# Kernel tuning notes

Measured on AMD Instinct MI355X. Metric: run time of the kernel, lower is better.

The kernel has to match this reference:

```python
import jax, jax.numpy as jnp
import numpy as np

N = 50000   # nodes
E = 800000  # edges (avg degree 16)
DIMS = [(128, 128), (128, 128), (128, 64)]  # (in, out) per SAGEConv layer
EPS_BN = 1e-5
EPS_NORM = 1e-12


def _make_layer(key, din, dout):
    k1, k2 = jax.random.split(key)
    s = 1.0 / np.sqrt(din)
    return (
        jax.random.normal(k1, (dout, din), jnp.float32) * s,  # Wl: neighbor linear
        jnp.zeros((dout,), jnp.float32),                      # bl
        jax.random.normal(k2, (dout, din), jnp.float32) * s,  # Wr: root linear (no bias in PyG)
        jnp.ones((dout,), jnp.float32),                       # bn gamma
        jnp.zeros((dout,), jnp.float32),                      # bn beta
        jnp.zeros((dout,), jnp.float32),                      # bn running mean
        jnp.ones((dout,), jnp.float32),                       # bn running var
    )


def setup_inputs() -> dict:
    key = jax.random.key(0)
    kx, ke, k0, k1, k2 = jax.random.split(key, 5)
    inp = {
        "x": jax.random.normal(kx, (N, 128), jnp.float32),
        "edge_index": jax.random.randint(ke, (2, E), 0, N, dtype=jnp.int32),
    }
    for i, (k, (din, dout)) in enumerate(zip([k0, k1, k2], DIMS)):
        Wl, bl, Wr, g, b, rm, rv = _make_layer(k, din, dout)
        inp.update({f"Wl{i}": Wl, f"bl{i}": bl, f"Wr{i}": Wr,
                    f"g{i}": g, f"b{i}": b, f"rm{i}": rm, f"rv{i}": rv})
    return inp


def _sage_conv(x, src, dst, Wl, bl, Wr):
    # mean aggregation of incoming messages: gather src features, scatter-add at dst
    agg = jax.ops.segment_sum(x[src], dst, num_segments=N)          # [N, din]
    deg = jax.ops.segment_sum(jnp.ones((src.shape[0],), x.dtype), dst, num_segments=N)
    mean = agg / jnp.maximum(deg, 1.0)[:, None]
    return mean @ Wl.T + bl + x @ Wr.T


def _bn_eval(x, g, b, rm, rv):
    return g * (x - rm) * jax.lax.rsqrt(rv + EPS_BN) + b


def reference(x, edge_index,
              Wl0, bl0, Wr0, g0, b0, rm0, rv0,
              Wl1, bl1, Wr1, g1, b1, rm1, rv1,
              Wl2, bl2, Wr2, g2, b2, rm2, rv2):
    src, dst = edge_index[0], edge_index[1]
    layers = [
        (Wl0, bl0, Wr0, g0, b0, rm0, rv0),
        (Wl1, bl1, Wr1, g1, b1, rm1, rv1),
        (Wl2, bl2, Wr2, g2, b2, rm2, rv2),
    ]
    h = x
    for i, (Wl, bl, Wr, g, b, rm, rv) in enumerate(layers):
        h = _bn_eval(_sage_conv(h, src, dst, Wl, bl, Wr), g, b, rm, rv)
        if i < len(layers) - 1:
            h = jax.nn.relu(h)  # dropout is identity in eval mode
    # F.normalize(p=2, dim=1)
    return h / jnp.maximum(jnp.linalg.norm(h, axis=1, keepdims=True), EPS_NORM)
```

## Files before the change

kernel.cpp:

```cpp
#include <hip/hip_runtime.h>
#include <hip/hip_bf16.h>

#define CDIV(a,b) (((a)+(b)-1)/(b))
#define NBUCK_MAX 512
#define FUSE_CAP 1536
#define CAPL     4096
#define AGGF_CAP 2048

typedef __attribute__((ext_vector_type(8))) short short8;
typedef __attribute__((ext_vector_type(4))) float f32x4;
typedef __attribute__((ext_vector_type(2))) float f32x2;

static __device__ __forceinline__ unsigned short f2bf(float f){
  union { float f; unsigned u; } v; v.f = f;
  unsigned r = v.u + 0x7fffu + ((v.u >> 16) & 1u);
  return (unsigned short)(r >> 16);
}
static __device__ __forceinline__ unsigned pack2(float lo, float hi){
  return (unsigned)f2bf(lo) | ((unsigned)f2bf(hi) << 16);
}
static __device__ __forceinline__ float bf2f(unsigned short s){
  union { unsigned u; float f; } v; v.u = ((unsigned)s) << 16; return v.f;
}
static __device__ __forceinline__ unsigned pk_fp8x4(float a, float b, float c, float d){
  int v = __builtin_amdgcn_cvt_pk_fp8_f32(a, b, 0, false);
  v = __builtin_amdgcn_cvt_pk_fp8_f32(c, d, v, true);
  return (unsigned)v;
}

#define ACCP16(v) { b0 += __builtin_amdgcn_cvt_pk_f32_fp8((int)v.x, false); \
                    b1 += __builtin_amdgcn_cvt_pk_f32_fp8((int)v.x, true);  \
                    b2 += __builtin_amdgcn_cvt_pk_f32_fp8((int)v.y, false); \
                    b3 += __builtin_amdgcn_cvt_pk_f32_fp8((int)v.y, true);  \
                    b4 += __builtin_amdgcn_cvt_pk_f32_fp8((int)v.z, false); \
                    b5 += __builtin_amdgcn_cvt_pk_f32_fp8((int)v.z, true);  \
                    b6 += __builtin_amdgcn_cvt_pk_f32_fp8((int)v.w, false); \
                    b7 += __builtin_amdgcn_cvt_pk_f32_fp8((int)v.w, true); }


struct WtpArgs {
  const float *W0, *W1, *bl, *g, *b, *rm, *rv;
  unsigned short* Bpk; float *sc; float *sh;
  int kblk, dout, do_bn, nblk, perm;
};

static __device__ __forceinline__ void wtp_one(const WtpArgs& a, int idx){
  int NB16 = a.kblk*32*a.dout;
  if (idx < NB16){
    int j = idx & 7, lane = (idx >> 3) & 63, rest = idx >> 9;
    int NT = a.dout >> 4;
    int nt = rest % NT, kk = rest / NT;
    int nn = nt*16 + (lane & 15);
    int k  = kk*32 + ((lane >> 4) * 8) + j;
    float v;
    if (k < 128){
      int kc = a.perm ? (((k & 7) << 4) | (k >> 3)) : k;
      v = a.W0[nn*128 + kc];
    } else {
      v = a.W1[nn*128 + (k - 128)];
    }
    a.Bpk[idx] = f2bf(v);
  } else if (a.do_bn && idx < NB16 + a.dout){
    int jj = idx - NB16;
    float s = a.g[jj] * rsqrtf(a.rv[jj] + 1e-5f);
    a.sc[jj] = s;
    a.sh[jj] = (a.bl[jj] - a.rm[jj]) * s + a.b[jj];
  }
}


__global__ __launch_bounds__(256) void k_prep(const float* __restrict__ x, int n4, unsigned* __restrict__ xb,
                                              unsigned* __restrict__ xq,
                                              const int* __restrict__ dst, int E,
                                              int* __restrict__ bcnt, int nbuck,
                                              int castBlocks, int histBlocks,
                                              WtpArgs a0, WtpArgs a1, WtpArgs a2, WtpArgs a3){
  __shared__ int s[NBUCK_MAX];
  int b = blockIdx.x, t = threadIdx.x;
  if (b < castBlocks){
    int i = b*256 + t;
    if (i < n4){
      float4 v = ((const float4*)x)[i];
      uint2 o; o.x = pack2(v.x, v.y); o.y = pack2(v.z, v.w);
      ((uint2*)xb)[i] = o;
      xq[i] = pk_fp8x4(v.x, v.y, v.z, v.w);
    }
    return;
  }
  b -= castBlocks;
  if (b < histBlocks){
    for (int i=t;i<nbuck;i+=256) s[i] = 0;
    __syncthreads();
    constexpr int EPT = 16;
    int e0 = b*256*EPT;
    #pragma unroll
    for (int i=0;i<EPT;i++){
      int e = e0 + i*256 + t;
      if (e < E) atomicAdd(&s[dst[e] >> 7], 1);
    }
    __syncthreads();
    for (int i=t;i<nbuck;i+=256){
      int c = s[i];
      if (c > 0) atomicAdd(&bcnt[i], c);
    }
    return;
  }
  b -= histBlocks;
  if (b < a0.nblk){ wtp_one(a0, b*256 + t); return; }
  b -= a0.nblk;
  if (b < a1.nblk){ wtp_one(a1, b*256 + t); return; }
  b -= a1.nblk;
  if (b < a2.nblk){ wtp_one(a2, b*256 + t); return; }
  b -= a2.nblk;
  wtp_one(a3, b*256 + t);
}

__global__ __launch_bounds__(256) void k_bucketA(const int* __restrict__ src, const int* __restrict__ dst,
                                                 int E, const int* __restrict__ bcnt,
                                                 int* __restrict__ bcur, unsigned* __restrict__ ebuf, int nbuck){
  __shared__ int scnt[NBUCK_MAX];
  __shared__ int sbase[NBUCK_MAX];
  __shared__ int sboff[NBUCK_MAX];
  __shared__ int ss[256];
  int t = threadIdx.x;
  {
    int a0 = (2*t   < nbuck) ? bcnt[2*t]   : 0;
    int a1 = (2*t+1 < nbuck) ? bcnt[2*t+1] : 0;
    ss[t] = a0 + a1; __syncthreads();
    for (int d=1; d<256; d<<=1){
      int u = (t>=d) ? ss[t-d] : 0;
      __syncthreads();
      ss[t] += u;
      __syncthreads();
    }
    int excl = ss[t] - (a0 + a1);
    if (2*t   < nbuck) sboff[2*t]   = excl;
    if (2*t+1 < nbuck) sboff[2*t+1] = excl + a0;
  }
  for (int i=t;i<nbuck;i+=256) scnt[i] = 0;
  __syncthreads();
  constexpr int EPT = 16;
  int e0 = blockIdx.x*256*EPT;
  int b[EPT]; unsigned pk[EPT];
  #pragma unroll
  for (int i=0;i<EPT;i++){
    int e = e0 + i*256 + t;
    if (e < E){
      int d = dst[e];
      b[i] = d >> 7;
      pk[i] = ((unsigned)(d & 127) << 16) | (unsigned)src[e];
      atomicAdd(&scnt[b[i]], 1);
    } else b[i] = -1;
  }
  __syncthreads();
  for (int i=t;i<nbuck;i+=256){
    int c = scnt[i];
    sbase[i] = (c > 0) ? atomicAdd(&bcur[i], c) : 0;
    scnt[i] = 0;
  }
  __syncthreads();
  #pragma unroll
  for (int i=0;i<EPT;i++){
    if (b[i] >= 0){
      int p = atomicAdd(&scnt[b[i]], 1);
      ebuf[(size_t)sboff[b[i]] + sbase[b[i]] + p] = pk[i];
    }
  }
}


__global__ __launch_bounds__(256, 3) void k_bfuse(
    const unsigned* __restrict__ ebuf, const int* __restrict__ bcnt, int nbuck, int E, int N,
    int* __restrict__ off, int* __restrict__ csr,
    const uint4* __restrict__ xq4, const unsigned short* __restrict__ Ag,
    const unsigned short* __restrict__ Bpk, const float* __restrict__ sc, const float* __restrict__ sh,
    unsigned short* __restrict__ outh, unsigned* __restrict__ outq){
  __shared__ uint4 Ms4[64*17];
  __shared__ int scsr[FUSE_CAP];
  __shared__ int sEx[NBUCK_MAX];
  __shared__ int ss[256];
  unsigned short* Ms = (unsigned short*)Ms4;
  int* sdeg = (int*)Ms4;
  int* sabs = sdeg + 128;
  int* cur  = sabs + 129;
  int bb_ = blockIdx.x;
  int b = bb_ >> 1, hi = bb_ & 1;
  int t = threadIdx.x;
  {
    int a0 = (2*t   < nbuck) ? bcnt[2*t]   : 0;
    int a1 = (2*t+1 < nbuck) ? bcnt[2*t+1] : 0;
    ss[t] = a0 + a1; __syncthreads();
    for (int d=1; d<256; d<<=1){
      int u = (t>=d) ? ss[t-d] : 0;
      __syncthreads();
      ss[t] += u;
      __syncthreads();
    }
    int excl = ss[t] - (a0 + a1);
    if (2*t   < nbuck) sEx[2*t]   = excl;
    if (2*t+1 < nbuck) sEx[2*t+1] = excl + a0;
  }
  if (t < 128){ sdeg[t] = 0; cur[t] = 0; }
  __syncthreads();
  int e0 = sEx[b];
  int e1 = (b+1 < nbuck) ? sEx[b+1] : E;
  for (int e = e0 + t; e < e1; e += 256)
    atomicAdd(&sdeg[ebuf[e] >> 16], 1);
  __syncthreads();
  for (int d=1; d<128; d<<=1){
    int u = (t < 128 && t >= d) ? sdeg[t-d] : 0;
    __syncthreads();
    if (t < 128) sdeg[t] += u;
    __syncthreads();
  }
  if (t == 0) sabs[0] = 0;
  if (t < 128) sabs[t+1] = sdeg[t];
  __syncthreads();
  int base64 = sabs[hi*64];
  int myTot  = sabs[hi*64 + 64] - base64;
  int n0 = (b << 7) + hi*64;
  int cnt = (N > n0) ? min(64, N - n0) : 0;
  if (cnt > 0 && t <= cnt) off[n0 + t] = e0 + sabs[hi*64 + t];
  int lane = t & 63, w = t >> 6, sl = lane & 7;
  int gs0[2], gs1[2];
  #pragma unroll
  for (int it=0; it<2; it++){
    int rk = w*16 + it*8 + (lane >> 3);
    gs0[it] = sabs[hi*64 + rk] - base64;
    gs1[it] = sabs[hi*64 + rk + 1] - base64;
  }
  bool fits = myTot <= FUSE_CAP;
  for (int e = e0 + t; e < e1; e += 256){
    unsigned pr = ebuf[e];
    int ln = (int)(pr >> 16);
    if ((ln >> 6) == hi){
      int p = atomicAdd(&cur[ln], 1);
      int gpos = sabs[ln] + p;
      int sv = (int)(pr & 0xffffu);
      if (fits) scsr[gpos - base64] = sv;
      else      csr[e0 + gpos] = sv;
    }
  }
  __syncthreads();
  const int* gcsr = csr + e0 + base64;
  if (fits){
    for (int i = t; i < myTot; i += 256) csr[e0 + base64 + i] = scsr[i];
  } else {
    for (int i = t; i < FUSE_CAP; i += 256) scsr[i] = gcsr[i];
    __syncthreads();
  }

  #pragma unroll
  for (int it=0; it<2; it++){
    int rk = w*16 + it*8 + (lane >> 3);
    int s0 = gs0[it], s1 = gs1[it];
    f32x2 b0={0,0},b1={0,0},b2={0,0},b3={0,0},b4={0,0},b5={0,0},b6={0,0},b7={0,0};
    int e = s0;
    for (; e + 8 <= s1; e += 8){
      int i0,i1,i2,i3,i4,i5,i6,i7;
      if (e + 8 <= FUSE_CAP){
        i0 = scsr[e];   i1 = scsr[e+1]; i2 = scsr[e+2]; i3 = scsr[e+3];
        i4 = scsr[e+4]; i5 = scsr[e+5]; i6 = scsr[e+6]; i7 = scsr[e+7];
      } else {
        i0 = gcsr[e];   i1 = gcsr[e+1]; i2 = gcsr[e+2]; i3 = gcsr[e+3];
        i4 = gcsr[e+4]; i5 = gcsr[e+5]; i6 = gcsr[e+6]; i7 = gcsr[e+7];
      }
      uint4 v0 = xq4[(size_t)i0*8 + sl];
      uint4 v1 = xq4[(size_t)i1*8 + sl];
      uint4 v2 = xq4[(size_t)i2*8 + sl];
      uint4 v3 = xq4[(size_t)i3*8 + sl];
      uint4 v4 = xq4[(size_t)i4*8 + sl];
      uint4 v5 = xq4[(size_t)i5*8 + sl];
      uint4 v6 = xq4[(size_t)i6*8 + sl];
      uint4 v7 = xq4[(size_t)i7*8 + sl];
      ACCP16(v0); ACCP16(v1); ACCP16(v2); ACCP16(v3);
      ACCP16(v4); ACCP16(v5); ACCP16(v6); ACCP16(v7);
    }
    for (; e + 4 <= s1; e += 4){
      int i0,i1,i2,i3;
      if (e + 4 <= FUSE_CAP){
        i0 = scsr[e]; i1 = scsr[e+1]; i2 = scsr[e+2]; i3 = scsr[e+3];
      } else {
        i0 = gcsr[e]; i1 = gcsr[e+1]; i2 = gcsr[e+2]; i3 = gcsr[e+3];
      }
      uint4 v0 = xq4[(size_t)i0*8 + sl];
      uint4 v1 = xq4[(size_t)i1*8 + sl];
      uint4 v2 = xq4[(size_t)i2*8 + sl];
      uint4 v3 = xq4[(size_t)i3*8 + sl];
      ACCP16(v0); ACCP16(v1); ACCP16(v2); ACCP16(v3);
    }
    for (; e < s1; e++){
      int ii = (e < FUSE_CAP) ? scsr[e] : gcsr[e];
      uint4 v = xq4[(size_t)ii*8 + sl];
      ACCP16(v);
    }
    int d = s1 - s0;
    float inv = 1.0f / (float)(d > 0 ? d : 1);
    uint4 o0, o1;
    o0.x = pack2(b0.x*inv, b0.y*inv);  o0.y = pack2(b1.x*inv, b1.y*inv);
    o0.z = pack2(b2.x*inv, b2.y*inv);  o0.w = pack2(b3.x*inv, b3.y*inv);
    o1.x = pack2(b4.x*inv, b4.y*inv);  o1.y = pack2(b5.x*inv, b5.y*inv);
    o1.z = pack2(b6.x*inv, b6.y*inv);  o1.w = pack2(b7.x*inv, b7.y*inv);
    Ms4[rk*17 + sl*2]     = o0;
    Ms4[rk*17 + sl*2 + 1] = o1;
  }
  __syncthreads();

  int quad = lane >> 4, c = lane & 15;
  int woff = w*16;
  int r0 = n0 + woff + c;

  f32x4 acc[8];
  #pragma unroll
  for (int nt=0;nt<8;nt++) acc[nt] = (f32x4){0.f,0.f,0.f,0.f};

  #pragma unroll
  for (int kk=0; kk<8; kk++){
    int ka = (kk & 3)*32 + quad*8;
    short8 a0;
    if (kk < 4){
      a0 = *(const short8*)&Ms[(woff + c)*136 + ka];
    } else {
      a0 = (short8){0,0,0,0,0,0,0,0};
      if (r0 < N) a0 = *(const short8*)(Ag + (size_t)r0*128 + ka);
    }
    #pragma unroll
    for (int nt=0; nt<8; nt++){
      short8 bb2 = *(const short8*)(Bpk + (size_t)((kk*8 + nt)*64 + lane)*8);
      acc[nt] = __builtin_amdgcn_mfma_f32_16x16x32_bf16(a0, bb2, acc[nt], 0, 0, 0);
    }
  }

  float scv[8], shv[8];
  #pragma unroll
  for (int nt=0;nt<8;nt++){ scv[nt] = sc[nt*16 + c]; shv[nt] = sh[nt*16 + c]; }

  #pragma unroll
  for (int r=0;r<4;r++){
    int row = n0 + woff + quad*4 + r;
    if (row < N){
      float u[8];
      #pragma unroll
      for (int nt=0;nt<8;nt++){
        float uu = acc[nt][r]*scv[nt] + shv[nt];
        u[nt] = fmaxf(uu, 0.f);
        outh[(size_t)row*128 + nt*16 + c] = f2bf(u[nt]);
      }
      uint2 q;
      q.x = pk_fp8x4(u[0], u[1], u[2], u[3]);
      q.y = pk_fp8x4(u[4], u[5], u[6], u[7]);
      ((uint2*)outq)[(size_t)row*16 + c] = q;
    }
  }
}


__global__ __launch_bounds__(256, 3) void k_fuse1(
    const uint4* __restrict__ hq4, const int* __restrict__ off, const int* __restrict__ csr,
    const unsigned short* __restrict__ Ag, const unsigned short* __restrict__ Bpk,
    const float* __restrict__ sc, const float* __restrict__ sh,
    const unsigned short* __restrict__ BpkL,
    unsigned short* __restrict__ outh, unsigned* __restrict__ outyl, int n){
  __shared__ uint4 Ms4[64*17];
  __shared__ uint4 sBL4[1024];
  __shared__ int sw[2];
  unsigned short* Ms = (unsigned short*)Ms4;
  int* scsr = (int*)sBL4;
  int t = threadIdx.x;
  int n0 = blockIdx.x*64;
  if (t < 2) sw[t] = off[min(n0 + t*64, n)];
  __syncthreads();
  int e0b = sw[0];
  int span = sw[1] - e0b;
  for (int i = t; i < span && i < CAPL; i += 256) scsr[i] = csr[e0b + i];
  __syncthreads();

  int lane = t & 63, w = t >> 6;
  int sl = lane & 7;

  #pragma unroll
  for (int it=0; it<2; it++){
    int rk = w*16 + it*8 + (lane >> 3);
    int idx = n0 + rk;
    bool valid = idx < n;
    int s0 = valid ? off[idx]   : 0;
    int s1 = valid ? off[idx+1] : 0;
    f32x2 b0={0,0},b1={0,0},b2={0,0},b3={0,0},b4={0,0},b5={0,0},b6={0,0},b7={0,0};
    int e = s0;
    for (; e + 8 <= s1; e += 8){
      int le = e - e0b;
      int i0,i1,i2,i3,i4,i5,i6,i7;
      if (le + 8 <= CAPL){
        i0 = scsr[le];   i1 = scsr[le+1]; i2 = scsr[le+2]; i3 = scsr[le+3];
        i4 = scsr[le+4]; i5 = scsr[le+5]; i6 = scsr[le+6]; i7 = scsr[le+7];
      } else {
        i0 = csr[e];   i1 = csr[e+1]; i2 = csr[e+2]; i3 = csr[e+3];
        i4 = csr[e+4]; i5 = csr[e+5]; i6 = csr[e+6]; i7 = csr[e+7];
      }
      uint4 v0 = hq4[(size_t)i0*8 + sl];
      uint4 v1 = hq4[(size_t)i1*8 + sl];
      uint4 v2 = hq4[(size_t)i2*8 + sl];
      uint4 v3 = hq4[(size_t)i3*8 + sl];
      uint4 v4 = hq4[(size_t)i4*8 + sl];
      uint4 v5 = hq4[(size_t)i5*8 + sl];
      uint4 v6 = hq4[(size_t)i6*8 + sl];
      uint4 v7 = hq4[(size_t)i7*8 + sl];
      ACCP16(v0); ACCP16(v1); ACCP16(v2); ACCP16(v3);
      ACCP16(v4); ACCP16(v5); ACCP16(v6); ACCP16(v7);
    }
    for (; e + 4 <= s1; e += 4){
      int le = e - e0b;
      int i0,i1,i2,i3;
      if (le + 4 <= CAPL){
        i0 = scsr[le]; i1 = scsr[le+1]; i2 = scsr[le+2]; i3 = scsr[le+3];
      } else {
        i0 = csr[e]; i1 = csr[e+1]; i2 = csr[e+2]; i3 = csr[e+3];
      }
      uint4 v0 = hq4[(size_t)i0*8 + sl];
      uint4 v1 = hq4[(size_t)i1*8 + sl];
      uint4 v2 = hq4[(size_t)i2*8 + sl];
      uint4 v3 = hq4[(size_t)i3*8 + sl];
      ACCP16(v0); ACCP16(v1); ACCP16(v2); ACCP16(v3);
    }
    for (; e < s1; e++){
      int le = e - e0b;
      int ii = (le < CAPL) ? scsr[le] : csr[e];
      uint4 v = hq4[(size_t)ii*8 + sl];
      ACCP16(v);
    }
    int d = s1 - s0;
    float inv = 1.0f / (float)(d > 0 ? d : 1);
    uint4 o0, o1;
    o0.x = pack2(b0.x*inv, b0.y*inv);  o0.y = pack2(b1.x*inv, b1.y*inv);
    o0.z = pack2(b2.x*inv, b2.y*inv);  o0.w = pack2(b3.x*inv, b3.y*inv);
    o1.x = pack2(b4.x*inv, b4.y*inv);  o1.y = pack2(b5.x*inv, b5.y*inv);
    o1.z = pack2(b6.x*inv, b6.y*inv);  o1.w = pack2(b7.x*inv, b7.y*inv);
    Ms4[rk*17 + sl*2]     = o0;
    Ms4[rk*17 + sl*2 + 1] = o1;
  }
  __syncthreads();

  int quad = lane >> 4, c = lane & 15;
  int woff = w*16;
  int r0 = n0 + woff + c;

  f32x4 acc[8];
  #pragma unroll
  for (int nt=0;nt<8;nt++) acc[nt] = (f32x4){0.f,0.f,0.f,0.f};

  #pragma unroll
  for (int kk=0; kk<8; kk++){
    int ka = (kk & 3)*32 + quad*8;
    short8 a0;
    if (kk < 4){
      a0 = *(const short8*)&Ms[(woff + c)*136 + ka];
    } else {
      a0 = (short8){0,0,0,0,0,0,0,0};
      if (r0 < n) a0 = *(const short8*)(Ag + (size_t)r0*128 + ka);
    }
    #pragma unroll
    for (int nt=0; nt<8; nt++){
      short8 bb2 = *(const short8*)(Bpk + (size_t)((kk*8 + nt)*64 + lane)*8);
      acc[nt] = __builtin_amdgcn_mfma_f32_16x16x32_bf16(a0, bb2, acc[nt], 0, 0, 0);
    }
  }

  float scv[8], shv[8];
  #pragma unroll
  for (int nt=0;nt<8;nt++){ scv[nt] = sc[nt*16 + c]; shv[nt] = sh[nt*16 + c]; }

  __syncthreads();

  #pragma unroll
  for (int r=0;r<4;r++){
    int lrow = woff + quad*4 + r;
    int row = n0 + lrow;
    if (row < n){
      float u[8];
      #pragma unroll
      for (int nt=0;nt<8;nt++){
        float uu = acc[nt][r]*scv[nt] + shv[nt];
        u[nt] = fmaxf(uu, 0.f);
        outh[(size_t)row*128 + nt*16 + c] = f2bf(u[nt]);
      }
      #pragma unroll
      for (int nt=0;nt<8;nt++) Ms[lrow*136 + nt*16 + c] = f2bf(u[nt]);
    } else {
      #pragma unroll
      for (int nt=0;nt<8;nt++) Ms[lrow*136 + nt*16 + c] = 0;
    }
  }

  {
    const uint4* sL = (const uint4*)BpkL;
    #pragma unroll
    for (int i=0;i<4;i++) sBL4[i*256 + t] = sL[i*256 + t];
  }
  __syncthreads();
  unsigned short* BsL = (unsigned short*)sBL4;
  f32x4 acc2[4];
  #pragma unroll
  for (int nt=0;nt<4;nt++) acc2[nt] = (f32x4){0.f,0.f,0.f,0.f};
  int r0l = woff + c;
  #pragma unroll
  for (int kk=0; kk<4; kk++){
    int ka = kk*32 + quad*8;
    short8 a0 = *(const short8*)&Ms[r0l*136 + ka];
    #pragma unroll
    for (int nt=0; nt<4; nt++){
      short8 bb2 = *(const short8*)&BsL[(size_t)((kk*4 + nt)*64 + lane)*8];
      acc2[nt] = __builtin_amdgcn_mfma_f32_16x16x32_bf16(a0, bb2, acc2[nt], 0, 0, 0);
    }
  }
  #pragma unroll
  for (int r=0;r<4;r++){
    int row = n0 + woff + quad*4 + r;
    if (row < n){
      unsigned q = pk_fp8x4(acc2[0][r], acc2[1][r], acc2[2][r], acc2[3][r]);
      outyl[(size_t)row*16 + c] = q;
    }
  }
}


__global__ __launch_bounds__(256, 3) void k_aggf(
    const uint4* __restrict__ ylq4, const int* __restrict__ off, const int* __restrict__ csr,
    const unsigned short* __restrict__ A0, const unsigned short* __restrict__ BpkR,
    const float* __restrict__ sc, const float* __restrict__ sh,
    float* __restrict__ outf, int n){
  __shared__ unsigned short Ms[64*64];
  __shared__ unsigned short Bs[128*64];
  __shared__ int scsr[AGGF_CAP];
  __shared__ int sw[2];
  int t = threadIdx.x;
  int n0 = blockIdx.x*64;
  if (t < 2) sw[t] = off[min(n0 + t*64, n)];
  {
    const uint4* s = (const uint4*)BpkR;
    uint4* d = (uint4*)Bs;
    #pragma unroll
    for (int i=0;i<4;i++) d[i*256 + t] = s[i*256 + t];
  }
  __syncthreads();
  int e0b = sw[0];
  int span = sw[1] - e0b;
  for (int i = t; i < span && i < AGGF_CAP; i += 256) scsr[i] = csr[e0b + i];
  __syncthreads();

  int lane = t & 63, w = t >> 6;
  int sl4 = lane & 3;

  {
    int rk = w*16 + (lane >> 2);
    int idx = n0 + rk;
    bool valid = idx < n;
    int s0 = valid ? off[idx]   : 0;
    int s1 = valid ? off[idx+1] : 0;
    f32x2 b0={0,0},b1={0,0},b2={0,0},b3={0,0},b4={0,0},b5={0,0},b6={0,0},b7={0,0};
    int e = s0;
    for (; e + 8 <= s1; e += 8){
      int le = e - e0b;
      int i0,i1,i2,i3,i4,i5,i6,i7;
      if (le + 8 <= AGGF_CAP){
        i0 = scsr[le];   i1 = scsr[le+1]; i2 = scsr[le+2]; i3 = scsr[le+3];
        i4 = scsr[le+4]; i5 = scsr[le+5]; i6 = scsr[le+6]; i7 = scsr[le+7];
      } else {
        i0 = csr[e];   i1 = csr[e+1]; i2 = csr[e+2]; i3 = csr[e+3];
        i4 = csr[e+4]; i5 = csr[e+5]; i6 = csr[e+6]; i7 = csr[e+7];
      }
      uint4 v0 = ylq4[(size_t)i0*4 + sl4];
      uint4 v1 = ylq4[(size_t)i1*4 + sl4];
      uint4 v2 = ylq4[(size_t)i2*4 + sl4];
      uint4 v3 = ylq4[(size_t)i3*4 + sl4];
      uint4 v4 = ylq4[(size_t)i4*4 + sl4];
      uint4 v5 = ylq4[(size_t)i5*4 + sl4];
      uint4 v6 = ylq4[(size_t)i6*4 + sl4];
      uint4 v7 = ylq4[(size_t)i7*4 + sl4];
      ACCP16(v0); ACCP16(v1); ACCP16(v2); ACCP16(v3);
      ACCP16(v4); ACCP16(v5); ACCP16(v6); ACCP16(v7);
    }
    for (; e + 4 <= s1; e += 4){
      int le = e - e0b;
      int i0,i1,i2,i3;
      if (le + 4 <= AGGF_CAP){
        i0 = scsr[le]; i1 = scsr[le+1]; i2 = scsr[le+2]; i3 = scsr[le+3];
      } else {
        i0 = csr[e]; i1 = csr[e+1]; i2 = csr[e+2]; i3 = csr[e+3];
      }
      uint4 v0 = ylq4[(size_t)i0*4 + sl4];
      uint4 v1 = ylq4[(size_t)i1*4 + sl4];
      uint4 v2 = ylq4[(size_t)i2*4 + sl4];
      uint4 v3 = ylq4[(size_t)i3*4 + sl4];
      ACCP16(v0); ACCP16(v1); ACCP16(v2); ACCP16(v3);
    }
    for (; e < s1; e++){
      int le = e - e0b;
      int ii = (le < AGGF_CAP) ? scsr[le] : csr[e];
      uint4 v = ylq4[(size_t)ii*4 + sl4];
      ACCP16(v);
    }
    int d = s1 - s0;
    float inv = 1.0f / (float)(d > 0 ? d : 1);
    uint4 o0, o1;
    o0.x = pack2(b0.x*inv, b0.y*inv);  o0.y = pack2(b1.x*inv, b1.y*inv);
    o0.z = pack2(b2.x*inv, b2.y*inv);  o0.w = pack2(b3.x*inv, b3.y*inv);
    o1.x = pack2(b4.x*inv, b4.y*inv);  o1.y = pack2(b5.x*inv, b5.y*inv);
    o1.z = pack2(b6.x*inv, b6.y*inv);  o1.w = pack2(b7.x*inv, b7.y*inv);
    ((uint4*)Ms)[rk*8 + sl4*2]     = o0;
    ((uint4*)Ms)[rk*8 + sl4*2 + 1] = o1;
  }
  __syncthreads();

  int quad = lane >> 4, c = lane & 15;
  int woff = w*16;
  int r0 = n0 + woff + c;
  f32x4 acc[4];
  #pragma unroll
  for (int nt=0;nt<4;nt++) acc[nt] = (f32x4){0.f,0.f,0.f,0.f};
  #pragma unroll
  for (int kk=0; kk<4; kk++){
    int ka = kk*32 + quad*8;
    short8 a0 = {0,0,0,0,0,0,0,0};
    if (r0 < n) a0 = *(const short8*)(A0 + (size_t)r0*128 + ka);
    #pragma unroll
    for (int nt=0; nt<4; nt++){
      short8 bb2 = *(const short8*)&Bs[(size_t)((kk*4 + nt)*64 + lane)*8];
      acc[nt] = __builtin_amdgcn_mfma_f32_16x16x32_bf16(a0, bb2, acc[nt], 0, 0, 0);
    }
  }

  float scv[4], shv[4];
  #pragma unroll
  for (int nt=0;nt<4;nt++){ scv[nt] = sc[nt*16 + c]; shv[nt] = sh[nt*16 + c]; }

  #pragma unroll
  for (int r=0;r<4;r++){
    int lr = woff + quad*4 + r;
    int row = n0 + lr;
    float v[4];
    float ss2 = 0.f;
    if (row < n){
      #pragma unroll
      for (int nt=0;nt<4;nt++){
        float u = acc[nt][r] + bf2f(Ms[lr*64 + c*4 + nt]);
        u = u*scv[nt] + shv[nt];
        v[nt] = u;
        ss2 += u*u;
      }
    } else {
      #pragma unroll
      for (int nt=0;nt<4;nt++) v[nt] = 0.f;
    }
    ss2 += __shfl_xor(ss2, 1, 64);
    ss2 += __shfl_xor(ss2, 2, 64);
    ss2 += __shfl_xor(ss2, 4, 64);
    ss2 += __shfl_xor(ss2, 8, 64);
    float rn = 1.0f / fmaxf(sqrtf(ss2), 1e-12f);
    if (row < n){
      #pragma unroll
      for (int nt=0;nt<4;nt++) outf[(size_t)row*64 + nt*16 + c] = v[nt]*rn;
    }
  }
}


extern "C" void kernel_launch(void* const* d_in, const int* in_sizes, int n_in,
                              void* d_out, int out_size, void* d_ws, size_t ws_size,
                              hipStream_t stream){
  const float* x = (const float*)d_in[0];
  const int* ei  = (const int*)d_in[1];
  int N = in_sizes[0] / 128;
  int E = in_sizes[1] / 2;
  const int* esrc = ei;
  const int* edst = ei + E;
  int nbuck = CDIV(N, 128);
  int nb2 = 2*nbuck;

  const float *Wl[3], *bl[3], *Wr[3], *g[3], *bb[3], *rm[3], *rv[3];
  int dout[3];
  for (int i=0;i<3;i++){
    int base = 2 + 7*i;
    Wl[i]=(const float*)d_in[base];   bl[i]=(const float*)d_in[base+1];
    Wr[i]=(const float*)d_in[base+2]; g[i] =(const float*)d_in[base+3];
    bb[i]=(const float*)d_in[base+4]; rm[i]=(const float*)d_in[base+5];
    rv[i]=(const float*)d_in[base+6];
    dout[i] = in_sizes[base] / 128;
  }

  char* p = (char*)d_ws;
  size_t o = 0;
  auto alloc = [&](size_t bytes)->void*{ void* r = p + o; o += (bytes + 255) & ~(size_t)255; return r; };
  int* bz    = (int*)alloc((size_t)2*nbuck*4);
  int* bcnt  = bz;
  int* bcur  = bz + nbuck;
  int* off   = (int*)alloc((size_t)(N+1)*4);
  int* csr   = (int*)alloc((size_t)E*4);
  unsigned* ebuf = (unsigned*)alloc((size_t)E*4);
  unsigned* xb   = (unsigned*)alloc((size_t)N*64*4);
  unsigned* xq   = (unsigned*)alloc((size_t)N*128);
  unsigned* h_a  = (unsigned*)alloc((size_t)N*64*4);
  unsigned* haq  = (unsigned*)alloc((size_t)N*128);
  unsigned* h_b  = (unsigned*)alloc((size_t)N*64*4);
  unsigned* ylb  = (unsigned*)alloc((size_t)N*64);
  unsigned short* Bpk01[2];
  float* sc[3]; float* sh[3];
  for (int i=0;i<2;i++) Bpk01[i] = (unsigned short*)alloc((size_t)256*dout[i]*2);
  unsigned short* BpkL = (unsigned short*)alloc((size_t)128*dout[2]*2);
  unsigned short* BpkR = (unsigned short*)alloc((size_t)128*dout[2]*2);
  for (int i=0;i<3;i++){
    sc[i] = (float*)alloc((size_t)dout[i]*4);
    sh[i] = (float*)alloc((size_t)dout[i]*4);
  }

  hipMemsetAsync(bz, 0, (size_t)2*nbuck*4, stream);

  WtpArgs wa[4];
  wa[0] = { Wl[0], Wr[0], bl[0], g[0], bb[0], rm[0], rv[0], Bpk01[0], sc[0], sh[0], 8, dout[0], 1, CDIV(256*dout[0]+dout[0],256), 0 };
  wa[1] = { Wl[1], Wr[1], bl[1], g[1], bb[1], rm[1], rv[1], Bpk01[1], sc[1], sh[1], 8, dout[1], 1, CDIV(256*dout[1]+dout[1],256), 1 };
  wa[2] = { Wl[2], nullptr, nullptr, nullptr, nullptr, nullptr, nullptr, BpkL, nullptr, nullptr, 4, dout[2], 0, CDIV(128*dout[2],256), 0 };
  wa[3] = { Wr[2], nullptr, bl[2], g[2], bb[2], rm[2], rv[2], BpkR, sc[2], sh[2], 4, dout[2], 1, CDIV(128*dout[2]+dout[2],256), 0 };

  int castBlocks = CDIV(N*32, 256);
  int histBlocks = CDIV(E, 256*16);
  int prepBlocks = castBlocks + histBlocks + wa[0].nblk + wa[1].nblk + wa[2].nblk + wa[3].nblk;
  k_prep   <<<prepBlocks,256,0,stream>>>(x, N*32, xb, xq, edst, E, bcnt, nbuck, castBlocks, histBlocks,
                                         wa[0], wa[1], wa[2], wa[3]);
  k_bucketA<<<CDIV(E,256*16),256,0,stream>>>(esrc, edst, E, bcnt, bcur, ebuf, nbuck);

  k_bfuse<<<nb2,256,0,stream>>>(ebuf, bcnt, nbuck, E, N, off, csr,
                                (const uint4*)xq, (const unsigned short*)xb,
                                Bpk01[0], sc[0], sh[0],
                                (unsigned short*)h_a, haq);
  k_fuse1<<<nb2,256,0,stream>>>((const uint4*)haq, off, csr,
                                (const unsigned short*)h_a, Bpk01[1], sc[1], sh[1], BpkL,
                                (unsigned short*)h_b, ylb, N);
  k_aggf<<<nb2,256,0,stream>>>((const uint4*)ylb, off, csr,
                               (const unsigned short*)h_b, BpkR, sc[2], sh[2],
                               (float*)d_out, N);
}
```

Measured before the change: 226.0 us.

## Bin edges into fixed-capacity buckets in prep, dropping the histogram pass and bucket kernel

Edges are now scattered straight into fixed-size per-bucket slots (BUCK_CAP entries per 128-node bucket) inside the prep kernel. A global overflow list catches buckets that exceed capacity. This removes the separate histogram pass, the k_bucketA launch and the prefix scans over bucket counts. Because CSR offsets are no longer contiguous, a per-node degree array is added and downstream kernels read off+deg. The cost is a padded CSR and edge buffer, plus every bfuse block scanning the whole overflow list, which gets slow if many buckets overflow.

```diff
diff --git a/kernel.cpp b/kernel.cpp
--- a/kernel.cpp
+++ b/kernel.cpp
@@ -3,6 +3,7 @@
 
 #define CDIV(a,b) (((a)+(b)-1)/(b))
 #define NBUCK_MAX 512
+#define BUCK_CAP 3072
 #define FUSE_CAP 1536
 #define CAPL     4096
 #define AGGF_CAP 2048
@@ -71,11 +72,13 @@
 
 __global__ __launch_bounds__(256) void k_prep(const float* __restrict__ x, int n4, unsigned* __restrict__ xb,
                                               unsigned* __restrict__ xq,
-                                              const int* __restrict__ dst, int E,
-                                              int* __restrict__ bcnt, int nbuck,
-                                              int castBlocks, int histBlocks,
+                                              const int* __restrict__ esrc, const int* __restrict__ edst,
+                                              int E, int* __restrict__ bcur, int* __restrict__ ovCnt,
+                                              unsigned* __restrict__ ebuf, unsigned* __restrict__ ovBuf,
+                                              int nbuck, int castBlocks, int binBlocks,
                                               WtpArgs a0, WtpArgs a1, WtpArgs a2, WtpArgs a3){
-  __shared__ int s[NBUCK_MAX];
+  __shared__ int scnt[NBUCK_MAX];
+  __shared__ int sbase[NBUCK_MAX];
   int b = blockIdx.x, t = threadIdx.x;
   if (b < castBlocks){
     int i = b*256 + t;
@@ -88,24 +91,41 @@
     return;
   }
   b -= castBlocks;
-  if (b < histBlocks){
-    for (int i=t;i<nbuck;i+=256) s[i] = 0;
+  if (b < binBlocks){
+    for (int i=t;i<nbuck;i+=256) scnt[i] = 0;
     __syncthreads();
     constexpr int EPT = 16;
     int e0 = b*256*EPT;
+    int bb[EPT]; unsigned pk[EPT];
     #pragma unroll
     for (int i=0;i<EPT;i++){
       int e = e0 + i*256 + t;
-      if (e < E) atomicAdd(&s[dst[e] >> 7], 1);
+      if (e < E){
+        int d = edst[e];
+        bb[i] = d >> 7;
+        pk[i] = ((unsigned)(d & 127) << 16) | (unsigned)esrc[e];
+        atomicAdd(&scnt[bb[i]], 1);
+      } else bb[i] = -1;
     }
     __syncthreads();
     for (int i=t;i<nbuck;i+=256){
-      int c = s[i];
-      if (c > 0) atomicAdd(&bcnt[i], c);
+      int c = scnt[i];
+      sbase[i] = (c > 0) ? atomicAdd(&bcur[i], c) : 0;
+      scnt[i] = 0;
+    }
+    __syncthreads();
+    #pragma unroll
+    for (int i=0;i<EPT;i++){
+      if (bb[i] >= 0){
+        int p = atomicAdd(&scnt[bb[i]], 1);
+        int gpos = sbase[bb[i]] + p;
+        if (gpos < BUCK_CAP) ebuf[(size_t)bb[i]*BUCK_CAP + gpos] = pk[i];
+        else { int oi = atomicAdd(ovCnt, 1); ovBuf[oi] = ((unsigned)bb[i] << 23) | pk[i]; }
+      }
     }
     return;
   }
-  b -= histBlocks;
+  b -= binBlocks;
   if (b < a0.nblk){ wtp_one(a0, b*256 + t); return; }
   b -= a0.nblk;
   if (b < a1.nblk){ wtp_one(a1, b*256 + t); return; }
@@ -115,97 +135,34 @@
   wtp_one(a3, b*256 + t);
 }
 
-__global__ __launch_bounds__(256) void k_bucketA(const int* __restrict__ src, const int* __restrict__ dst,
-                                                 int E, const int* __restrict__ bcnt,
-                                                 int* __restrict__ bcur, unsigned* __restrict__ ebuf, int nbuck){
-  __shared__ int scnt[NBUCK_MAX];
-  __shared__ int sbase[NBUCK_MAX];
-  __shared__ int sboff[NBUCK_MAX];
-  __shared__ int ss[256];
-  int t = threadIdx.x;
-  {
-    int a0 = (2*t   < nbuck) ? bcnt[2*t]   : 0;
-    int a1 = (2*t+1 < nbuck) ? bcnt[2*t+1] : 0;
-    ss[t] = a0 + a1; __syncthreads();
-    for (int d=1; d<256; d<<=1){
-      int u = (t>=d) ? ss[t-d] : 0;
-      __syncthreads();
-      ss[t] += u;
-      __syncthreads();
-    }
-    int excl = ss[t] - (a0 + a1);
-    if (2*t   < nbuck) sboff[2*t]   = excl;
-    if (2*t+1 < nbuck) sboff[2*t+1] = excl + a0;
-  }
-  for (int i=t;i<nbuck;i+=256) scnt[i] = 0;
-  __syncthreads();
-  constexpr int EPT = 16;
-  int e0 = blockIdx.x*256*EPT;
-  int b[EPT]; unsigned pk[EPT];
-  #pragma unroll
-  for (int i=0;i<EPT;i++){
-    int e = e0 + i*256 + t;
-    if (e < E){
-      int d = dst[e];
-      b[i] = d >> 7;
-      pk[i] = ((unsigned)(d & 127) << 16) | (unsigned)src[e];
-      atomicAdd(&scnt[b[i]], 1);
-    } else b[i] = -1;
-  }
-  __syncthreads();
-  for (int i=t;i<nbuck;i+=256){
-    int c = scnt[i];
-    sbase[i] = (c > 0) ? atomicAdd(&bcur[i], c) : 0;
-    scnt[i] = 0;
-  }
-  __syncthreads();
-  #pragma unroll
-  for (int i=0;i<EPT;i++){
-    if (b[i] >= 0){
-      int p = atomicAdd(&scnt[b[i]], 1);
-      ebuf[(size_t)sboff[b[i]] + sbase[b[i]] + p] = pk[i];
-    }
-  }
-}
-
 
 __global__ __launch_bounds__(256, 3) void k_bfuse(
-    const unsigned* __restrict__ ebuf, const int* __restrict__ bcnt, int nbuck, int E, int N,
-    int* __restrict__ off, int* __restrict__ csr,
+    const unsigned* __restrict__ ebuf, const int* __restrict__ bcur,
+    const int* __restrict__ ovCnt, const unsigned* __restrict__ ovBuf, int N,
+    int* __restrict__ off, int* __restrict__ deg, int* __restrict__ csr,
     const uint4* __restrict__ xq4, const unsigned short* __restrict__ Ag,
     const unsigned short* __restrict__ Bpk, const float* __restrict__ sc, const float* __restrict__ sh,
     unsigned short* __restrict__ outh, unsigned* __restrict__ outq){
   __shared__ uint4 Ms4[64*17];
   __shared__ int scsr[FUSE_CAP];
-  __shared__ int sEx[NBUCK_MAX];
-  __shared__ int ss[256];
   unsigned short* Ms = (unsigned short*)Ms4;
   int* sdeg = (int*)Ms4;
   int* sabs = sdeg + 128;
   int* cur  = sabs + 129;
-  int bb_ = blockIdx.x;
-  int b = bb_ >> 1, hi = bb_ & 1;
+  int wb = blockIdx.x;
+  int b = wb >> 1, hi = wb & 1;
   int t = threadIdx.x;
-  {
-    int a0 = (2*t   < nbuck) ? bcnt[2*t]   : 0;
-    int a1 = (2*t+1 < nbuck) ? bcnt[2*t+1] : 0;
-    ss[t] = a0 + a1; __syncthreads();
-    for (int d=1; d<256; d<<=1){
-      int u = (t>=d) ? ss[t-d] : 0;
-      __syncthreads();
-      ss[t] += u;
-      __syncthreads();
-    }
-    int excl = ss[t] - (a0 + a1);
-    if (2*t   < nbuck) sEx[2*t]   = excl;
-    if (2*t+1 < nbuck) sEx[2*t+1] = excl + a0;
-  }
   if (t < 128){ sdeg[t] = 0; cur[t] = 0; }
   __syncthreads();
-  int e0 = sEx[b];
-  int e1 = (b+1 < nbuck) ? sEx[b+1] : E;
-  for (int e = e0 + t; e < e1; e += 256)
-    atomicAdd(&sdeg[ebuf[e] >> 16], 1);
+  size_t bBase = (size_t)b*BUCK_CAP;
+  int cntMain = min(bcur[b], BUCK_CAP);
+  int ov = *ovCnt;
+  for (int e = t; e < cntMain; e += 256)
+    atomicAdd(&sdeg[ebuf[bBase + e] >> 16], 1);
+  for (int i = t; i < ov; i += 256){
+    unsigned v = ovBuf[i];
+    if ((int)(v >> 23) == b) atomicAdd(&sdeg[(v >> 16) & 127u], 1);
+  }
   __syncthreads();
   for (int d=1; d<128; d<<=1){
     int u = (t < 128 && t >= d) ? sdeg[t-d] : 0;
@@ -220,7 +177,10 @@
   int myTot  = sabs[hi*64 + 64] - base64;
   int n0 = (b << 7) + hi*64;
   int cnt = (N > n0) ? min(64, N - n0) : 0;
-  if (cnt > 0 && t <= cnt) off[n0 + t] = e0 + sabs[hi*64 + t];
+  if (t < cnt){
+    off[n0 + t] = (int)bBase + sabs[hi*64 + t];
+    deg[n0 + t] = sabs[hi*64 + t + 1] - sabs[hi*64 + t];
+  }
   int lane = t & 63, w = t >> 6, sl = lane & 7;
   int gs0[2], gs1[2];
   #pragma unroll
@@ -230,21 +190,34 @@
     gs1[it] = sabs[hi*64 + rk + 1] - base64;
   }
   bool fits = myTot <= FUSE_CAP;
-  for (int e = e0 + t; e < e1; e += 256){
-    unsigned pr = ebuf[e];
+  for (int e = t; e < cntMain; e += 256){
+    unsigned pr = ebuf[bBase + e];
     int ln = (int)(pr >> 16);
     if ((ln >> 6) == hi){
       int p = atomicAdd(&cur[ln], 1);
       int gpos = sabs[ln] + p;
       int sv = (int)(pr & 0xffffu);
       if (fits) scsr[gpos - base64] = sv;
-      else      csr[e0 + gpos] = sv;
-    }
-  }
-  __syncthreads();
-  const int* gcsr = csr + e0 + base64;
+      else      csr[bBase + gpos] = sv;
+    }
+  }
+  for (int i = t; i < ov; i += 256){
+    unsigned v = ovBuf[i];
+    if ((int)(v >> 23) == b){
+      int ln = (int)((v >> 16) & 127u);
+      if ((ln >> 6) == hi){
+        int p = atomicAdd(&cur[ln], 1);
+        int gpos = sabs[ln] + p;
+        int sv = (int)(v & 0xffffu);
+        if (fits) scsr[gpos - base64] = sv;
+        else      csr[bBase + gpos] = sv;
+      }
+    }
+  }
+  __syncthreads();
+  const int* gcsr = csr + bBase + base64;
   if (fits){
-    for (int i = t; i < myTot; i += 256) csr[e0 + base64 + i] = scsr[i];
+    for (int i = t; i < myTot; i += 256) csr[bBase + base64 + i] = scsr[i];
   } else {
     for (int i = t; i < FUSE_CAP; i += 256) scsr[i] = gcsr[i];
     __syncthreads();
@@ -356,7 +329,8 @@
 
 
 __global__ __launch_bounds__(256, 3) void k_fuse1(
-    const uint4* __restrict__ hq4, const int* __restrict__ off, const int* __restrict__ csr,
+    const uint4* __restrict__ hq4, const int* __restrict__ off, const int* __restrict__ deg,
+    const int* __restrict__ csr,
     const unsigned short* __restrict__ Ag, const unsigned short* __restrict__ Bpk,
     const float* __restrict__ sc, const float* __restrict__ sh,
     const unsigned short* __restrict__ BpkL,
@@ -368,7 +342,11 @@
   int* scsr = (int*)sBL4;
   int t = threadIdx.x;
   int n0 = blockIdx.x*64;
-  if (t < 2) sw[t] = off[min(n0 + t*64, n)];
+  if (t == 0){
+    sw[0] = off[n0];
+    int last = min(n0 + 63, n - 1);
+    sw[1] = off[last] + deg[last];
+  }
   __syncthreads();
   int e0b = sw[0];
   int span = sw[1] - e0b;
@@ -383,8 +361,8 @@
     int rk = w*16 + it*8 + (lane >> 3);
     int idx = n0 + rk;
     bool valid = idx < n;
-    int s0 = valid ? off[idx]   : 0;
-    int s1 = valid ? off[idx+1] : 0;
+    int s0 = valid ? off[idx] : 0;
+    int s1 = valid ? (s0 + deg[idx]) : 0;
     f32x2 b0={0,0},b1={0,0},b2={0,0},b3={0,0},b4={0,0},b5={0,0},b6={0,0},b7={0,0};
     int e = s0;
     for (; e + 8 <= s1; e += 8){
@@ -524,7 +502,8 @@
 
 
 __global__ __launch_bounds__(256, 3) void k_aggf(
-    const uint4* __restrict__ ylq4, const int* __restrict__ off, const int* __restrict__ csr,
+    const uint4* __restrict__ ylq4, const int* __restrict__ off, const int* __restrict__ deg,
+    const int* __restrict__ csr,
     const unsigned short* __restrict__ A0, const unsigned short* __restrict__ BpkR,
     const float* __restrict__ sc, const float* __restrict__ sh,
     float* __restrict__ outf, int n){
@@ -534,7 +513,11 @@
   __shared__ int sw[2];
   int t = threadIdx.x;
   int n0 = blockIdx.x*64;
-  if (t < 2) sw[t] = off[min(n0 + t*64, n)];
+  if (t == 0){
+    sw[0] = off[n0];
+    int last = min(n0 + 63, n - 1);
+    sw[1] = off[last] + deg[last];
+  }
   {
     const uint4* s = (const uint4*)BpkR;
     uint4* d = (uint4*)Bs;
@@ -554,8 +537,8 @@
     int rk = w*16 + (lane >> 2);
     int idx = n0 + rk;
     bool valid = idx < n;
-    int s0 = valid ? off[idx]   : 0;
-    int s1 = valid ? off[idx+1] : 0;
+    int s0 = valid ? off[idx] : 0;
+    int s1 = valid ? (s0 + deg[idx]) : 0;
     f32x2 b0={0,0},b1={0,0},b2={0,0},b3={0,0},b4={0,0},b5={0,0},b6={0,0},b7={0,0};
     int e = s0;
     for (; e + 8 <= s1; e += 8){
@@ -690,12 +673,14 @@
   char* p = (char*)d_ws;
   size_t o = 0;
   auto alloc = [&](size_t bytes)->void*{ void* r = p + o; o += (bytes + 255) & ~(size_t)255; return r; };
-  int* bz    = (int*)alloc((size_t)2*nbuck*4);
-  int* bcnt  = bz;
-  int* bcur  = bz + nbuck;
-  int* off   = (int*)alloc((size_t)(N+1)*4);
-  int* csr   = (int*)alloc((size_t)E*4);
-  unsigned* ebuf = (unsigned*)alloc((size_t)E*4);
+  int* bz    = (int*)alloc((size_t)(nbuck + 1)*4);
+  int* bcur  = bz;
+  int* ovCnt = bz + nbuck;
+  int* off   = (int*)alloc((size_t)N*4);
+  int* deg   = (int*)alloc((size_t)N*4);
+  int* csr   = (int*)alloc((size_t)nbuck*BUCK_CAP*4);
+  unsigned* ebuf  = (unsigned*)alloc((size_t)nbuck*BUCK_CAP*4);
+  unsigned* ovBuf = (unsigned*)alloc((size_t)E*4);
   unsigned* xb   = (unsigned*)alloc((size_t)N*64*4);
   unsigned* xq   = (unsigned*)alloc((size_t)N*128);
   unsigned* h_a  = (unsigned*)alloc((size_t)N*64*4);
@@ -712,7 +697,7 @@
     sh[i] = (float*)alloc((size_t)dout[i]*4);
   }
 
-  hipMemsetAsync(bz, 0, (size_t)2*nbuck*4, stream);
+  hipMemsetAsync(bz, 0, (size_t)(nbuck + 1)*4, stream);
 
   WtpArgs wa[4];
   wa[0] = { Wl[0], Wr[0], bl[0], g[0], bb[0], rm[0], rv[0], Bpk01[0], sc[0], sh[0], 8, dout[0], 1, CDIV(256*dout[0]+dout[0],256), 0 };
@@ -721,20 +706,20 @@
   wa[3] = { Wr[2], nullptr, bl[2], g[2], bb[2], rm[2], rv[2], BpkR, sc[2], sh[2], 4, dout[2], 1, CDIV(128*dout[2]+dout[2],256), 0 };
 
   int castBlocks = CDIV(N*32, 256);
-  int histBlocks = CDIV(E, 256*16);
-  int prepBlocks = castBlocks + histBlocks + wa[0].nblk + wa[1].nblk + wa[2].nblk + wa[3].nblk;
-  k_prep   <<<prepBlocks,256,0,stream>>>(x, N*32, xb, xq, edst, E, bcnt, nbuck, castBlocks, histBlocks,
-                                         wa[0], wa[1], wa[2], wa[3]);
-  k_bucketA<<<CDIV(E,256*16),256,0,stream>>>(esrc, edst, E, bcnt, bcur, ebuf, nbuck);
-
-  k_bfuse<<<nb2,256,0,stream>>>(ebuf, bcnt, nbuck, E, N, off, csr,
+  int binBlocks  = CDIV(E, 256*16);
+  int prepBlocks = castBlocks + binBlocks + wa[0].nblk + wa[1].nblk + wa[2].nblk + wa[3].nblk;
+  k_prep<<<prepBlocks,256,0,stream>>>(x, N*32, xb, xq, esrc, edst, E, bcur, ovCnt, ebuf, ovBuf,
+                                      nbuck, castBlocks, binBlocks,
+                                      wa[0], wa[1], wa[2], wa[3]);
+
+  k_bfuse<<<nb2,256,0,stream>>>(ebuf, bcur, ovCnt, ovBuf, N, off, deg, csr,
                                 (const uint4*)xq, (const unsigned short*)xb,
                                 Bpk01[0], sc[0], sh[0],
                                 (unsigned short*)h_a, haq);
-  k_fuse1<<<nb2,256,0,stream>>>((const uint4*)haq, off, csr,
+  k_fuse1<<<nb2,256,0,stream>>>((const uint4*)haq, off, deg, csr,
                                 (const unsigned short*)h_a, Bpk01[1], sc[1], sh[1], BpkL,
                                 (unsigned short*)h_b, ylb, N);
-  k_aggf<<<nb2,256,0,stream>>>((const uint4*)ylb, off, csr,
+  k_aggf<<<nb2,256,0,stream>>>((const uint4*)ylb, off, deg, csr,
                                (const unsigned short*)h_b, BpkR, sc[2], sh[2],
                                (float*)d_out, N);
 }
```

Result: faster. 216.7 us (-4.1%).
